# Optimization experiments

Measured on AMD Instinct MI355X. Metric: run time of the kernel, lower is better.

## Reference

```python
import jax, jax.numpy as jnp
import numpy as np

N, L, E, H = 2, 2048, 1024, 16
DH = E // H  # head_dim = 64


def setup_inputs() -> dict:
    key = jax.random.key(0)
    ks = jax.random.split(key, 11)
    s_h = 1.0 / np.sqrt(DH)
    s_e = 1.0 / np.sqrt(E)
    return {
        "EP_q": jax.random.normal(ks[0], (N, L, E), jnp.float32),
        "EP_k": jax.random.normal(ks[1], (N, L, E), jnp.float32),
        "EP_v": jax.random.normal(ks[2], (N, L, E), jnp.float32),
        "W_q": jax.random.uniform(ks[3], (DH, DH), jnp.float32, -s_h, s_h),
        "b_q": jax.random.uniform(ks[4], (DH,), jnp.float32, -s_h, s_h),
        "W_k": jax.random.uniform(ks[5], (DH, DH), jnp.float32, -s_h, s_h),
        "b_k": jax.random.uniform(ks[6], (DH,), jnp.float32, -s_h, s_h),
        "W_v": jax.random.uniform(ks[7], (DH, DH), jnp.float32, -s_h, s_h),
        "b_v": jax.random.uniform(ks[8], (DH,), jnp.float32, -s_h, s_h),
        "W_o": jax.random.uniform(ks[9], (E, E), jnp.float32, -s_e, s_e),
        "b_o": jax.random.uniform(ks[10], (E,), jnp.float32, -s_e, s_e),
    }


def reference(EP_q, EP_k, EP_v, W_q, b_q, W_k, b_k, W_v, b_v, W_o, b_o):
    n, q_len = EP_q.shape[0], EP_q.shape[1]
    # split into heads: (N, L, H, DH)
    q = EP_q.reshape(n, q_len, H, DH)
    k = EP_k.reshape(n, EP_k.shape[1], H, DH)
    v = EP_v.reshape(n, EP_v.shape[1], H, DH)
    # per-head linear (same weights across heads), torch Linear: x @ W.T + b
    Q = q @ W_q.T + b_q
    K = k @ W_k.T + b_k
    V = v @ W_v.T + b_v
    # scores (N, H, Lq, Lk); NOTE: scaled by sqrt(embed_size) per original code
    scores = jnp.einsum("nqhd,nkhd->nhqk", Q, K) / jnp.sqrt(jnp.float32(E))
    attn = jax.nn.softmax(scores, axis=-1)
    out = jnp.einsum("nhqk,nkhd->nqhd", attn, V).reshape(n, q_len, E)
    return out @ W_o.T + b_o
```

## Files before the change

kernel.cpp:

```cpp
#include <hip/hip_runtime.h>

#define N_B 2
#define L_L 2048
#define E_E 1024
#define H_H 16
#define D_H 64
#define LDSP 72

typedef __bf16 bf16x8 __attribute__((ext_vector_type(8)));
typedef float f32x4 __attribute__((ext_vector_type(4)));
typedef short s16x8 __attribute__((ext_vector_type(8)));
typedef unsigned short u16x4 __attribute__((ext_vector_type(4)));

__device__ __forceinline__ f32x4 mfma16(bf16x8 a, bf16x8 b, f32x4 c) {
  return __builtin_amdgcn_mfma_f32_16x16x32_bf16(a, b, c, 0, 0, 0);
}

__device__ __forceinline__ unsigned short f2bf(float x) {
  unsigned int u = __float_as_uint(x);
  u = (u + 0x7fffu + ((u >> 16) & 1u)) >> 16;
  return (unsigned short)u;
}

__device__ __forceinline__ unsigned int cvtpk(float lo, float hi) {
  unsigned int r;
  asm("v_cvt_pk_bf16_f32 %0, %1, %2" : "=v"(r) : "v"(lo), "v"(hi));
  return r;
}

__device__ __forceinline__ void swap32(unsigned int& a, unsigned int& b) {
  asm("v_permlane32_swap_b32 %0, %1" : "+v"(a), "+v"(b));
}
__device__ __forceinline__ void swap16(unsigned int& a, unsigned int& b) {
  asm("v_permlane16_swap_b32 %0, %1" : "+v"(a), "+v"(b));
}

__device__ __forceinline__ float exp2a(float x) {
  float r;
  asm("v_exp_f32 %0, %1" : "=v"(r) : "v"(x));
  return r;
}

__device__ __forceinline__ void gload16(const void* g, void* l) {
  __builtin_amdgcn_global_load_lds(
      (__attribute__((address_space(1))) void*)g,
      (__attribute__((address_space(3))) void*)l, 16, 0, 0);
}

__device__ __forceinline__ bf16x8 pack_frag(float p0, float p1, float p2, float p3,
                                            float p4, float p5, float p6, float p7) {
  unsigned int x0 = cvtpk(p0, p1), x1 = cvtpk(p2, p3);
  unsigned int x2 = cvtpk(p4, p5), x3 = cvtpk(p6, p7);
  swap32(x0, x2); swap16(x0, x2);
  swap32(x1, x3); swap16(x1, x3);
  union { unsigned int u[4]; bf16x8 v; } f;
  f.u[0] = x0; f.u[1] = x1; f.u[2] = x2; f.u[3] = x3;
  return f.v;
}

__global__ __launch_bounds__(256) void qkv_gemm_kernel(
    const float* __restrict__ EPq, const float* __restrict__ EPk, const float* __restrict__ EPv,
    const float* __restrict__ Wq, const float* __restrict__ Wk, const float* __restrict__ Wv,
    const float* __restrict__ bq, const float* __restrict__ bk, const float* __restrict__ bv,
    const float* __restrict__ Wo, unsigned short* __restrict__ Wob,
    unsigned short* __restrict__ Qb, unsigned short* __restrict__ Kb,
    unsigned short* __restrict__ Vtb) {
  __shared__ __attribute__((aligned(16))) unsigned short Xs[64][LDSP];
  __shared__ __attribute__((aligned(16))) unsigned short Ws[64][LDSP];
  const int tid = threadIdx.x;
  const int wid = tid >> 6;
  const int lane = tid & 63;
  const int lr = lane & 15;
  const int lg = lane >> 4;
  const int nh = blockIdx.x >> 5;
  const int l0 = (blockIdx.x & 31) * 64;
  const int n = nh >> 4;
  const int h = nh & 15;
  const float SCQ = 0.03125f * 1.44269504089f;

  {
    const int i = blockIdx.x * 256 + tid;
    const float4 f = ((const float4*)Wo)[i];
    u16x4 v = { f2bf(f.x), f2bf(f.y), f2bf(f.z), f2bf(f.w) };
    *(u16x4*)&Wob[(size_t)i * 4] = v;
  }

  #pragma unroll
  for (int mat = 0; mat < 3; ++mat) {
    const float* X = (mat == 0) ? EPq : (mat == 1) ? EPk : EPv;
    const float* W = (mat == 0) ? Wq : (mat == 1) ? Wk : Wv;
    const float* bias = (mat == 0) ? bq : (mat == 1) ? bk : bv;
    const float osc = (mat == 0) ? SCQ : 1.0f;

    const float* xb = X + ((size_t)(n * L_L + l0)) * E_E + h * D_H;
    #pragma unroll
    for (int it = 0; it < 4; ++it) {
      const int idx = it * 256 + tid;
      const int row = idx >> 4, c = idx & 15;
      const float4 f = *(const float4*)(xb + (size_t)row * E_E + c * 4);
      u16x4 v = { f2bf(f.x), f2bf(f.y), f2bf(f.z), f2bf(f.w) };
      *(u16x4*)&Xs[row][c * 4] = v;
    }
    #pragma unroll
    for (int it = 0; it < 4; ++it) {
      const int idx = it * 256 + tid;
      const int row = idx >> 4, c = idx & 15;
      const float4 f = *(const float4*)(W + idx * 4);
      u16x4 v = { f2bf(f.x), f2bf(f.y), f2bf(f.z), f2bf(f.w) };
      *(u16x4*)&Ws[row][c * 4] = v;
    }
    __syncthreads();

    const bf16x8 a0 = *(const bf16x8*)&Xs[wid * 16 + lr][lg * 8];
    const bf16x8 a1 = *(const bf16x8*)&Xs[wid * 16 + lr][32 + lg * 8];
    f32x4 acc[4];
    #pragma unroll
    for (int t = 0; t < 4; ++t) {
      const float bb = bias[t * 16 + lr];
      acc[t] = f32x4{bb, bb, bb, bb};
      const bf16x8 b0 = *(const bf16x8*)&Ws[t * 16 + lr][lg * 8];
      const bf16x8 b1 = *(const bf16x8*)&Ws[t * 16 + lr][32 + lg * 8];
      acc[t] = mfma16(a0, b0, acc[t]);
      acc[t] = mfma16(a1, b1, acc[t]);
    }
    __syncthreads();

    #pragma unroll
    for (int t = 0; t < 4; ++t)
      #pragma unroll
      for (int r = 0; r < 4; ++r)
        Xs[wid * 16 + lg * 4 + r][t * 16 + lr] = f2bf(acc[t][r] * osc);
    __syncthreads();

    if (mat < 2) {
      unsigned short* dst = ((mat == 0) ? Qb : Kb) + ((size_t)nh * L_L + l0) * D_H;
      #pragma unroll
      for (int it = 0; it < 2; ++it) {
        const int idx = it * 256 + tid;
        const int row = idx >> 3, c = idx & 7;
        *(s16x8*)(dst + (size_t)row * D_H + c * 8) = *(s16x8*)&Xs[row][c * 8];
      }
    } else {
      #pragma unroll
      for (int it = 0; it < 2; ++it) {
        const int idx = it * 256 + tid;
        const int d = idx & 63, c = idx >> 6;
        s16x8 v;
        #pragma unroll
        for (int j = 0; j < 8; ++j) v[j] = (short)Xs[c * 8 + j][d];
        *(s16x8*)(Vtb + ((size_t)nh * D_H + d) * L_L + l0 + c * 8) = v;
      }
    }
    __syncthreads();
  }
}

__global__ __launch_bounds__(256, 4) void attn_mfma_kernel(
    const unsigned short* __restrict__ Qb, const unsigned short* __restrict__ Kb,
    const unsigned short* __restrict__ Vtb, unsigned short* __restrict__ Ab) {
  __shared__ __attribute__((aligned(16))) unsigned short KS[2][64][64];
  __shared__ __attribute__((aligned(16))) unsigned short VS[2][64][64];

  const int tid = threadIdx.x;
  const int wid = tid >> 6;
  const int lane = tid & 63;
  const int lr = lane & 15;
  const int lg = lane >> 4;

  const int bid = ((blockIdx.x & 7) << 7) + (blockIdx.x >> 3);
  const int nh = bid >> 5;
  const int q0w = (bid & 31) * 64 + wid * 16;

  const unsigned short* gQ = Qb + ((size_t)nh * L_L + q0w) * D_H;
  const unsigned short* gK = Kb + (size_t)nh * L_L * D_H;
  const unsigned short* gV = Vtb + (size_t)nh * D_H * L_L;

  bf16x8 bQ[2];
  #pragma unroll
  for (int c2 = 0; c2 < 2; ++c2)
    bQ[c2] = *(const bf16x8*)(gQ + lr * D_H + c2 * 32 + lg * 8);

  const s16x8 ones16 = {0x3F80,0x3F80,0x3F80,0x3F80,0x3F80,0x3F80,0x3F80,0x3F80};
  const bf16x8 ones = *(const bf16x8*)&ones16;

  const int srow0 = tid >> 3, sch0 = tid & 7;
  const int srow1 = srow0 + 32;
  const int kc0 = (sch0 ^ (srow0 & 7)) * 8;
  const int kc1 = (sch0 ^ (srow1 & 7)) * 8;

  #define STAGE_K(buf, ktt)                                                    \
    do {                                                                       \
      unsigned short* kd = &KS[buf][0][0];                                     \
      gload16(gK + (size_t)((ktt) * 64 + srow0) * D_H + kc0,                   \
              kd + srow0 * 64 + sch0 * 8);                                     \
      gload16(gK + (size_t)((ktt) * 64 + srow1) * D_H + kc1,                   \
              kd + srow1 * 64 + sch0 * 8);                                     \
    } while (0)
  #define STAGE_V(buf, ktt)                                                    \
    do {                                                                       \
      unsigned short* vd = &VS[buf][0][0];                                     \
      gload16(gV + (size_t)srow0 * L_L + (ktt) * 64 + kc0,                     \
              vd + srow0 * 64 + sch0 * 8);                                     \
      gload16(gV + (size_t)srow1 * L_L + (ktt) * 64 + kc1,                     \
              vd + srow1 * 64 + sch0 * 8);                                     \
    } while (0)

  f32x4 acc[4] = {f32x4{0,0,0,0},f32x4{0,0,0,0},f32x4{0,0,0,0},f32x4{0,0,0,0}};
  f32x4 lacc = {0,0,0,0};
  f32x4 svA[4], svB[4];

  #define QKT(SV, kbuf)                                                        \
    do {                                                                       \
      const char* Kc = (const char*)&KS[kbuf][0][0];                           \
      __builtin_amdgcn_s_setprio(1);                                           \
      _Pragma("unroll")                                                        \
      for (int kb = 0; kb < 4; ++kb) {                                         \
        const int row = kb * 16 + lr;                                          \
        const bf16x8 a0 = *(const bf16x8*)(Kc + row * 128 + ((lg ^ (row & 7)) << 4)); \
        const bf16x8 a1 = *(const bf16x8*)(Kc + row * 128 + (((4 + lg) ^ (row & 7)) << 4)); \
        SV[kb] = mfma16(a1, bQ[1], mfma16(a0, bQ[0], f32x4{0,0,0,0}));         \
      }                                                                        \
      __builtin_amdgcn_s_setprio(0);                                           \
    } while (0)

  #define SMPV(SV, vbuf)                                                       \
    do {                                                                       \
      _Pragma("unroll")                                                        \
      for (int kb = 0; kb < 4; ++kb)                                           \
        _Pragma("unroll")                                                      \
        for (int r = 0; r < 4; ++r) SV[kb][r] = exp2a(SV[kb][r]);              \
      bf16x8 aP[2];                                                            \
      aP[0] = pack_frag(SV[0][0], SV[0][1], SV[0][2], SV[0][3],                \
                        SV[1][0], SV[1][1], SV[1][2], SV[1][3]);               \
      aP[1] = pack_frag(SV[2][0], SV[2][1], SV[2][2], SV[2][3],                \
                        SV[3][0], SV[3][1], SV[3][2], SV[3][3]);               \
      const char* Vc = (const char*)&VS[vbuf][0][0];                           \
      __builtin_amdgcn_s_setprio(1);                                           \
      lacc = mfma16(aP[0], ones, lacc); lacc = mfma16(aP[1], ones, lacc);      \
      _Pragma("unroll")                                                        \
      for (int t = 0; t < 4; ++t) {                                            \
        const int row = t * 16 + lr;                                           \
        const bf16x8 v0 = *(const bf16x8*)(Vc + row * 128 + ((lg ^ (row & 7)) << 4)); \
        const bf16x8 v1 = *(const bf16x8*)(Vc + row * 128 + (((4 + lg) ^ (row & 7)) << 4)); \
        acc[t] = mfma16(aP[0], v0, acc[t]);                                    \
        acc[t] = mfma16(aP[1], v1, acc[t]);                                    \
      }                                                                        \
      __builtin_amdgcn_s_setprio(0);                                           \
    } while (0)

  STAGE_K(0, 0);
  STAGE_K(1, 1);
  STAGE_V(0, 0);
  __syncthreads();
  QKT(svA, 0);
  __syncthreads();

  #pragma unroll 1
  for (int t2 = 0; t2 < 16; ++t2) {
    {
      const int t = 2 * t2;
      QKT(svB, 1);
      if (t2 < 15) STAGE_K(0, t + 2);
      STAGE_V(1, t + 1);
      SMPV(svA, 0);
      __syncthreads();
    }
    {
      const int t = 2 * t2 + 1;
      if (t2 < 15) {
        QKT(svA, 0);
        STAGE_K(1, t + 2);
        STAGE_V(0, t + 1);
      }
      SMPV(svB, 1);
      __syncthreads();
    }
  }
  #undef STAGE_K
  #undef STAGE_V
  #undef QKT
  #undef SMPV

  const int n = nh >> 4, h = nh & 15;
  f32x4 inv;
  #pragma unroll
  for (int r = 0; r < 4; ++r) inv[r] = 1.0f / lacc[r];
  #pragma unroll
  for (int t = 0; t < 4; ++t)
    #pragma unroll
    for (int r = 0; r < 4; ++r) {
      const int q = q0w + 4 * lg + r;
      Ab[((size_t)(n * L_L + q)) * E_E + h * D_H + t * 16 + lr] =
          f2bf(acc[t][r] * inv[r]);
    }
}

__global__ __launch_bounds__(256, 2) void out_gemm_kernel(
    const unsigned short* __restrict__ Ab, const unsigned short* __restrict__ Wob,
    const float* __restrict__ bo, float* __restrict__ out) {
  __shared__ __attribute__((aligned(16))) unsigned short As[2][64][64];
  __shared__ __attribute__((aligned(16))) unsigned short Bs[2][128][64];
  const int tid = threadIdx.x;
  const int wid = tid >> 6;
  const int lane = tid & 63;
  const int lr = lane & 15;
  const int lg = lane >> 4;

  const int bid = ((blockIdx.x & 7) << 6) + (blockIdx.x >> 3);
  const int m0 = (bid >> 3) * 64;
  const int n0 = (bid & 7) * 128;
  const int wr = wid >> 1, wc = wid & 1;

  const int r0 = tid >> 3, sc = tid & 7;
  const int scol = (sc ^ (r0 & 7)) * 8;

  #define OSTAGE(buf, kt)                                                      \
    do {                                                                       \
      unsigned short* ad = &As[buf][0][0];                                     \
      unsigned short* bd = &Bs[buf][0][0];                                     \
      gload16(Ab + (size_t)(m0 + r0) * E_E + (kt) * 64 + scol,                 \
              ad + r0 * 64 + sc * 8);                                          \
      gload16(Ab + (size_t)(m0 + r0 + 32) * E_E + (kt) * 64 + scol,            \
              ad + (r0 + 32) * 64 + sc * 8);                                   \
      gload16(Wob + (size_t)(n0 + r0) * E_E + (kt) * 64 + scol,                \
              bd + r0 * 64 + sc * 8);                                          \
      gload16(Wob + (size_t)(n0 + r0 + 32) * E_E + (kt) * 64 + scol,           \
              bd + (r0 + 32) * 64 + sc * 8);                                   \
      gload16(Wob + (size_t)(n0 + r0 + 64) * E_E + (kt) * 64 + scol,           \
              bd + (r0 + 64) * 64 + sc * 8);                                   \
      gload16(Wob + (size_t)(n0 + r0 + 96) * E_E + (kt) * 64 + scol,           \
              bd + (r0 + 96) * 64 + sc * 8);                                   \
    } while (0)

  f32x4 acc[2][4];
  #pragma unroll
  for (int mi = 0; mi < 2; ++mi)
    #pragma unroll
    for (int ni = 0; ni < 4; ++ni) {
      const float bb = bo[n0 + wc * 64 + ni * 16 + lr];
      acc[mi][ni] = f32x4{bb, bb, bb, bb};
    }

  OSTAGE(0, 0);
  __syncthreads();
  int cur = 0;

  for (int kt = 0; kt < 16; ++kt) {
    if (kt < 15) OSTAGE(cur ^ 1, kt + 1);

    const char* Ac = (const char*)&As[cur][0][0];
    const char* Bc = (const char*)&Bs[cur][0][0];
    bf16x8 af[2][2], bfr[4][2];
    #pragma unroll
    for (int mi = 0; mi < 2; ++mi) {
      const int row = wr * 32 + mi * 16 + lr;
      #pragma unroll
      for (int kb = 0; kb < 2; ++kb)
        af[mi][kb] = *(const bf16x8*)(Ac + row * 128 + (((kb * 4 + lg) ^ (row & 7)) << 4));
    }
    #pragma unroll
    for (int ni = 0; ni < 4; ++ni) {
      const int row = wc * 64 + ni * 16 + lr;
      #pragma unroll
      for (int kb = 0; kb < 2; ++kb)
        bfr[ni][kb] = *(const bf16x8*)(Bc + row * 128 + (((kb * 4 + lg) ^ (row & 7)) << 4));
    }
    __builtin_amdgcn_s_setprio(1);
    #pragma unroll
    for (int kb = 0; kb < 2; ++kb)
      #pragma unroll
      for (int mi = 0; mi < 2; ++mi)
        #pragma unroll
        for (int ni = 0; ni < 4; ++ni)
          acc[mi][ni] = mfma16(af[mi][kb], bfr[ni][kb], acc[mi][ni]);
    __builtin_amdgcn_s_setprio(0);

    __syncthreads();
    cur ^= 1;
  }
  #undef OSTAGE

  #pragma unroll
  for (int mi = 0; mi < 2; ++mi)
    #pragma unroll
    for (int ni = 0; ni < 4; ++ni) {
      const int nn = n0 + wc * 64 + ni * 16 + lr;
      #pragma unroll
      for (int r = 0; r < 4; ++r) {
        const int mm = m0 + wr * 32 + mi * 16 + lg * 4 + r;
        out[(size_t)mm * E_E + nn] = acc[mi][ni][r];
      }
    }
}

extern "C" void kernel_launch(void* const* d_in, const int* in_sizes, int n_in,
                              void* d_out, int out_size, void* d_ws, size_t ws_size,
                              hipStream_t stream) {
  const float* EPq = (const float*)d_in[0];
  const float* EPk = (const float*)d_in[1];
  const float* EPv = (const float*)d_in[2];
  const float* Wq  = (const float*)d_in[3];
  const float* bq  = (const float*)d_in[4];
  const float* Wk  = (const float*)d_in[5];
  const float* bk  = (const float*)d_in[6];
  const float* Wv  = (const float*)d_in[7];
  const float* bv  = (const float*)d_in[8];
  const float* Wo  = (const float*)d_in[9];
  const float* bo  = (const float*)d_in[10];
  float* out = (float*)d_out;

  unsigned short* ws = (unsigned short*)d_ws;
  const size_t SZ = (size_t)N_B * H_H * L_L * D_H;
  unsigned short* Qb  = ws;
  unsigned short* Kb  = Qb + SZ;
  unsigned short* Vtb = Kb + SZ;
  unsigned short* Ab  = Vtb + SZ;
  unsigned short* Wob = Ab + SZ;

  qkv_gemm_kernel<<<1024, 256, 0, stream>>>(
      EPq, EPk, EPv, Wq, Wk, Wv, bq, bk, bv, Wo, Wob, Qb, Kb, Vtb);
  attn_mfma_kernel<<<1024, 256, 0, stream>>>(Qb, Kb, Vtb, Ab);
  out_gemm_kernel<<<512, 256, 0, stream>>>(Ab, Wob, bo, out);
}
```

Before: 76.98 us.

## Process 32 query rows per wave in attention to reuse K/V fragments

Each wave now handles two 16-row query blocks instead of one, so a block covers 128 queries and the grid halves to 512 blocks. Every K and V fragment read from LDS feeds twice as many MFMAs, and each block stages K/V tiles for twice the queries, which cuts LDS and global traffic per unit of work. The cost is roughly double the register use for scores and accumulators, with launch bounds relaxed from 4 to 2 blocks per SM, and fewer blocks to hide latency and balance across CUs.

Measured after the change: 71.37 us (median of 3 runs). 7.3% less time.

```diff
diff --git a/kernel.cpp b/kernel.cpp
--- a/kernel.cpp
+++ b/kernel.cpp
@@ -47,10 +47,9 @@
       (__attribute__((address_space(3))) void*)l, 16, 0, 0);
 }
 
-__device__ __forceinline__ bf16x8 pack_frag(float p0, float p1, float p2, float p3,
-                                            float p4, float p5, float p6, float p7) {
-  unsigned int x0 = cvtpk(p0, p1), x1 = cvtpk(p2, p3);
-  unsigned int x2 = cvtpk(p4, p5), x3 = cvtpk(p6, p7);
+__device__ __forceinline__ bf16x8 pack_frag(const f32x4& plo, const f32x4& phi) {
+  unsigned int x0 = cvtpk(plo[0], plo[1]), x1 = cvtpk(plo[2], plo[3]);
+  unsigned int x2 = cvtpk(phi[0], phi[1]), x3 = cvtpk(phi[2], phi[3]);
   swap32(x0, x2); swap16(x0, x2);
   swap32(x1, x3); swap16(x1, x3);
   union { unsigned int u[4]; bf16x8 v; } f;
@@ -155,7 +154,7 @@
   }
 }
 
-__global__ __launch_bounds__(256, 4) void attn_mfma_kernel(
+__global__ __launch_bounds__(256, 2) void attn_mfma_kernel(
     const unsigned short* __restrict__ Qb, const unsigned short* __restrict__ Kb,
     const unsigned short* __restrict__ Vtb, unsigned short* __restrict__ Ab) {
   __shared__ __attribute__((aligned(16))) unsigned short KS[2][64][64];
@@ -167,18 +166,20 @@
   const int lr = lane & 15;
   const int lg = lane >> 4;
 
-  const int bid = ((blockIdx.x & 7) << 7) + (blockIdx.x >> 3);
-  const int nh = bid >> 5;
-  const int q0w = (bid & 31) * 64 + wid * 16;
+  const int bid = ((blockIdx.x & 7) << 6) + (blockIdx.x >> 3);
+  const int nh = bid >> 4;
+  const int q0w = ((bid & 15) << 7) + wid * 32;
 
   const unsigned short* gQ = Qb + ((size_t)nh * L_L + q0w) * D_H;
   const unsigned short* gK = Kb + (size_t)nh * L_L * D_H;
   const unsigned short* gV = Vtb + (size_t)nh * D_H * L_L;
 
-  bf16x8 bQ[2];
+  bf16x8 bQ[2][2];
   #pragma unroll
-  for (int c2 = 0; c2 < 2; ++c2)
-    bQ[c2] = *(const bf16x8*)(gQ + lr * D_H + c2 * 32 + lg * 8);
+  for (int qb = 0; qb < 2; ++qb)
+    #pragma unroll
+    for (int c2 = 0; c2 < 2; ++c2)
+      bQ[qb][c2] = *(const bf16x8*)(gQ + (qb * 16 + lr) * D_H + c2 * 32 + lg * 8);
 
   const s16x8 ones16 = {0x3F80,0x3F80,0x3F80,0x3F80,0x3F80,0x3F80,0x3F80,0x3F80};
   const bf16x8 ones = *(const bf16x8*)&ones16;
@@ -205,11 +206,12 @@
               vd + srow1 * 64 + sch0 * 8);                                     \
     } while (0)
 
-  f32x4 acc[4] = {f32x4{0,0,0,0},f32x4{0,0,0,0},f32x4{0,0,0,0},f32x4{0,0,0,0}};
-  f32x4 lacc = {0,0,0,0};
-  f32x4 svA[4], svB[4];
-
-  #define QKT(SV, kbuf)                                                        \
+  f32x4 acc0[4] = {f32x4{0,0,0,0},f32x4{0,0,0,0},f32x4{0,0,0,0},f32x4{0,0,0,0}};
+  f32x4 acc1[4] = {f32x4{0,0,0,0},f32x4{0,0,0,0},f32x4{0,0,0,0},f32x4{0,0,0,0}};
+  f32x4 lacc0 = {0,0,0,0}, lacc1 = {0,0,0,0};
+  f32x4 svA0[4], svA1[4], svB0[4], svB1[4];
+
+  #define QKT(SQ0, SQ1, kbuf)                                                  \
     do {                                                                       \
       const char* Kc = (const char*)&KS[kbuf][0][0];                           \
       __builtin_amdgcn_s_setprio(1);                                           \
@@ -218,32 +220,35 @@
         const int row = kb * 16 + lr;                                          \
         const bf16x8 a0 = *(const bf16x8*)(Kc + row * 128 + ((lg ^ (row & 7)) << 4)); \
         const bf16x8 a1 = *(const bf16x8*)(Kc + row * 128 + (((4 + lg) ^ (row & 7)) << 4)); \
-        SV[kb] = mfma16(a1, bQ[1], mfma16(a0, bQ[0], f32x4{0,0,0,0}));         \
+        SQ0[kb] = mfma16(a1, bQ[0][1], mfma16(a0, bQ[0][0], f32x4{0,0,0,0}));  \
+        SQ1[kb] = mfma16(a1, bQ[1][1], mfma16(a0, bQ[1][0], f32x4{0,0,0,0}));  \
       }                                                                        \
       __builtin_amdgcn_s_setprio(0);                                           \
     } while (0)
 
-  #define SMPV(SV, vbuf)                                                       \
+  #define SMPV(SQ0, SQ1, vbuf)                                                 \
     do {                                                                       \
       _Pragma("unroll")                                                        \
       for (int kb = 0; kb < 4; ++kb)                                           \
         _Pragma("unroll")                                                      \
-        for (int r = 0; r < 4; ++r) SV[kb][r] = exp2a(SV[kb][r]);              \
-      bf16x8 aP[2];                                                            \
-      aP[0] = pack_frag(SV[0][0], SV[0][1], SV[0][2], SV[0][3],                \
-                        SV[1][0], SV[1][1], SV[1][2], SV[1][3]);               \
-      aP[1] = pack_frag(SV[2][0], SV[2][1], SV[2][2], SV[2][3],                \
-                        SV[3][0], SV[3][1], SV[3][2], SV[3][3]);               \
+        for (int r = 0; r < 4; ++r) {                                          \
+          SQ0[kb][r] = exp2a(SQ0[kb][r]);                                      \
+          SQ1[kb][r] = exp2a(SQ1[kb][r]);                                      \
+        }                                                                      \
+      bf16x8 aP0[2], aP1[2];                                                   \
+      aP0[0] = pack_frag(SQ0[0], SQ0[1]); aP0[1] = pack_frag(SQ0[2], SQ0[3]);  \
+      aP1[0] = pack_frag(SQ1[0], SQ1[1]); aP1[1] = pack_frag(SQ1[2], SQ1[3]);  \
       const char* Vc = (const char*)&VS[vbuf][0][0];                           \
       __builtin_amdgcn_s_setprio(1);                                           \
-      lacc = mfma16(aP[0], ones, lacc); lacc = mfma16(aP[1], ones, lacc);      \
+      lacc0 = mfma16(aP0[0], ones, lacc0); lacc0 = mfma16(aP0[1], ones, lacc0);\
+      lacc1 = mfma16(aP1[0], ones, lacc1); lacc1 = mfma16(aP1[1], ones, lacc1);\
       _Pragma("unroll")                                                        \
       for (int t = 0; t < 4; ++t) {                                            \
         const int row = t * 16 + lr;                                           \
         const bf16x8 v0 = *(const bf16x8*)(Vc + row * 128 + ((lg ^ (row & 7)) << 4)); \
         const bf16x8 v1 = *(const bf16x8*)(Vc + row * 128 + (((4 + lg) ^ (row & 7)) << 4)); \
-        acc[t] = mfma16(aP[0], v0, acc[t]);                                    \
-        acc[t] = mfma16(aP[1], v1, acc[t]);                                    \
+        acc0[t] = mfma16(aP0[0], v0, acc0[t]); acc0[t] = mfma16(aP0[1], v1, acc0[t]); \
+        acc1[t] = mfma16(aP1[0], v0, acc1[t]); acc1[t] = mfma16(aP1[1], v1, acc1[t]); \
       }                                                                        \
       __builtin_amdgcn_s_setprio(0);                                           \
     } while (0)
@@ -252,27 +257,27 @@
   STAGE_K(1, 1);
   STAGE_V(0, 0);
   __syncthreads();
-  QKT(svA, 0);
+  QKT(svA0, svA1, 0);
   __syncthreads();
 
   #pragma unroll 1
   for (int t2 = 0; t2 < 16; ++t2) {
     {
       const int t = 2 * t2;
-      QKT(svB, 1);
+      QKT(svB0, svB1, 1);
       if (t2 < 15) STAGE_K(0, t + 2);
       STAGE_V(1, t + 1);
-      SMPV(svA, 0);
+      SMPV(svA0, svA1, 0);
       __syncthreads();
     }
     {
       const int t = 2 * t2 + 1;
       if (t2 < 15) {
-        QKT(svA, 0);
+        QKT(svA0, svA1, 0);
         STAGE_K(1, t + 2);
         STAGE_V(0, t + 1);
       }
-      SMPV(svB, 1);
+      SMPV(svB0, svB1, 1);
       __syncthreads();
     }
   }
@@ -282,17 +287,21 @@
   #undef SMPV
 
   const int n = nh >> 4, h = nh & 15;
-  f32x4 inv;
   #pragma unroll
-  for (int r = 0; r < 4; ++r) inv[r] = 1.0f / lacc[r];
-  #pragma unroll
-  for (int t = 0; t < 4; ++t)
-    #pragma unroll
-    for (int r = 0; r < 4; ++r) {
-      const int q = q0w + 4 * lg + r;
-      Ab[((size_t)(n * L_L + q)) * E_E + h * D_H + t * 16 + lr] =
-          f2bf(acc[t][r] * inv[r]);
-    }
+  for (int qb = 0; qb < 2; ++qb) {
+    const f32x4& la = qb ? lacc1 : lacc0;
+    f32x4* ac = qb ? acc1 : acc0;
+    f32x4 inv;
+    #pragma unroll
+    for (int r = 0; r < 4; ++r) inv[r] = 1.0f / la[r];
+    const int qbase = q0w + qb * 16 + 4 * lg;
+    #pragma unroll
+    for (int t = 0; t < 4; ++t)
+      #pragma unroll
+      for (int r = 0; r < 4; ++r)
+        Ab[((size_t)(n * L_L + qbase + r)) * E_E + h * D_H + t * 16 + lr] =
+            f2bf(ac[t][r] * inv[r]);
+  }
 }
 
 __global__ __launch_bounds__(256, 2) void out_gemm_kernel(
@@ -419,6 +428,6 @@
 
   qkv_gemm_kernel<<<1024, 256, 0, stream>>>(
       EPq, EPk, EPv, Wq, Wk, Wv, bq, bk, bv, Wo, Wob, Qb, Kb, Vtb);
-  attn_mfma_kernel<<<1024, 256, 0, stream>>>(Qb, Kb, Vtb, Ab);
+  attn_mfma_kernel<<<512, 256, 0, stream>>>(Qb, Kb, Vtb, Ab);
   out_gemm_kernel<<<512, 256, 0, stream>>>(Ab, Wob, bo, out);
 }
```
